# Optimization experiments

Hardware: AMD Instinct MI355X
Metric: run time of the kernel (lower is better)

The kernel has to match this reference:

```python
import jax, jax.numpy as jnp
import numpy as np

SR = 16000; NFFT = 1024; HOP = 256; NMELS = 80; GRUH = 256; ZDIM = 16
NBINS = 65; HID = 512; B = 8; TLEN = 160000; PAD = NFFT // 2; IRLEN = 8000

def _consts():
    freqs = np.linspace(0, SR / 2, NFFT // 2 + 1); fsq = freqs ** 2
    aw = (12194.217 ** 2 * fsq ** 2) / ((fsq + 20.6 ** 2) * (fsq + 107.7 ** 2) * (fsq + 737.9 ** 2) * (fsq + 12194.217 ** 2) ** 0.5 + 1e-8)
    h2m = lambda f: 2595.0 * np.log10(1.0 + f / 700.0)
    m2h = lambda m: 700.0 * (10.0 ** (m / 2595.0) - 1.0)
    f_pts = m2h(np.linspace(h2m(0.0), h2m(SR / 2.0), NMELS + 2))
    fd = f_pts[1:] - f_pts[:-1]
    sl = f_pts[None, :] - freqs[:, None]
    fb = np.maximum(0.0, np.minimum(-sl[:, :-2] / fd[:-1], sl[:, 2:] / fd[1:]))
    win = 0.5 - 0.5 * np.cos(2.0 * np.pi * np.arange(NFFT) / NFFT)  # periodic hann
    return jnp.asarray(aw, jnp.float32), jnp.asarray(fb, jnp.float32), jnp.asarray(win, jnp.float32)
AW, MELFB, WIN = _consts()

def _frame(x, size, hop):
    n = (x.shape[-1] - size) // hop + 1
    idx = jnp.arange(n)[:, None] * hop + jnp.arange(size)[None, :]
    return x[:, idx]

def _stft(x):  # [B,T] -> [B, n_frames, 513] complex
    xp = jnp.pad(x, ((0, 0), (PAD, PAD)), mode='reflect')
    return jnp.fft.rfft(_frame(xp, NFFT, HOP) * WIN, axis=-1)

def _istft(spec, length):  # [B, n_frames, 513] -> [B, length]
    fr = jnp.fft.irfft(spec, n=NFFT, axis=-1) * WIN
    n = fr.shape[1]; total = (n - 1) * HOP + NFFT
    idx = (jnp.arange(n)[:, None] * HOP + jnp.arange(NFFT)[None, :]).reshape(-1)
    out = jnp.zeros((fr.shape[0], total), fr.dtype).at[:, idx].add(fr.reshape(fr.shape[0], -1))
    wsq = jnp.zeros((total,), WIN.dtype).at[idx].add(jnp.tile(WIN ** 2, (n,)))
    out = out / jnp.where(wsq > 1e-11, wsq, 1.0)
    return out[:, PAD:PAD + length]

def _lin_interp(x, size):  # torch F.interpolate(mode='linear', align_corners=False) on last axis
    L = x.shape[-1]
    pos = jnp.clip((jnp.arange(size) + 0.5) * (L / size) - 0.5, 0.0, L - 1.0)
    lo = jnp.floor(pos).astype(jnp.int32); hi = jnp.minimum(lo + 1, L - 1); w = pos - lo
    return x[..., lo] * (1.0 - w) + x[..., hi] * w

def _gru(x, wih, whh, bih, bhh):  # torch nn.GRU, batch_first, h0=0
    xp = x @ wih.T + bih
    def step(h, xt):
        gh = h @ whh.T + bhh
        xr, xz, xn = jnp.split(xt, 3, -1); hr, hz, hn = jnp.split(gh, 3, -1)
        r = jax.nn.sigmoid(xr + hr); z = jax.nn.sigmoid(xz + hz)
        nn_ = jnp.tanh(xn + r * hn)
        h = (1.0 - z) * nn_ + z * h
        return h, h
    h0 = jnp.zeros((x.shape[0], whh.shape[1]), x.dtype)
    _, hs = jax.lax.scan(step, h0, jnp.swapaxes(xp, 0, 1))
    return jnp.swapaxes(hs, 0, 1)

def _forward(audio, gender, age, gru_wih, gru_whh, gru_bih, gru_bhh, proj_w, proj_b,
             w0, b0, g0, e0, w1, b1, g1, e1, w2, b2, g2, e2,
             oq_w, oq_b, vt_w, vt_b, nf_w, nf_b, ir):
    # --- pitch via autocorrelation ---
    xp = jnp.pad(audio, ((0, 0), (PAD, PAD)), mode='reflect')
    fr = _frame(xp, NFFT, HOP)
    ps = jnp.abs(jnp.fft.rfft(fr, n=2 * NFFT, axis=-1)) ** 2
    ac = jnp.fft.irfft(ps, n=2 * NFFT, axis=-1)[..., :NFFT]
    ac = ac / (ac[..., :1] + 1e-8)
    min_lag, max_lag = SR // 1000, SR // 50  # 16, 320
    reg = ac[..., min_lag:max_lag]
    mv = jnp.max(reg, -1); mi = jnp.argmax(reg, -1)
    f0 = SR / (mi.astype(jnp.float32) + min_lag + 1e-8)
    f0 = jnp.where(mv < 0.3, 0.0, f0)[..., None]  # [B,F,1]
    # --- loudness + mels ---
    spec = jnp.abs(_stft(audio)) ** 2  # [B,F,513]
    loud = 10.0 * jnp.log10(jnp.mean((spec + 1e-8) * AW, -1, keepdims=True))  # [B,F,1]
    mels = jnp.log(spec @ MELFB + 1e-5)  # [B,F,80]
    mels = (mels - mels.mean(1, keepdims=True)) / jnp.sqrt(mels.var(1, keepdims=True) + 1e-5)
    z = _gru(mels, gru_wih, gru_whh, gru_bih, gru_bhh) @ proj_w.T + proj_b  # [B,F,16]
    Fn = f0.shape[1]
    # --- controller ---
    gb = jnp.broadcast_to(gender[:, None, :], (gender.shape[0], Fn, 2))
    ab = jnp.broadcast_to(age[:, None, :], (age.shape[0], Fn, 1))
    h = jnp.concatenate([z, (jnp.log(f0 + 1e-5) - 4.0) / 4.0, loud / 100.0 + 1.0, gb, ab], -1)
    for W, bb, gm, bt in ((w0, b0, g0, e0), (w1, b1, g1, e1), (w2, b2, g2, e2)):
        h = h @ W.T + bb
        h = (h - h.mean(-1, keepdims=True)) / jnp.sqrt(h.var(-1, keepdims=True) + 1e-5) * gm + bt
        h = jnp.where(h >= 0, h, 0.1 * h)  # LeakyReLU(0.1)
    oq = jax.nn.sigmoid(h @ oq_w.T + oq_b)
    vt = jax.nn.sigmoid(h @ vt_w.T + vt_b)
    nf = jax.nn.sigmoid(h @ nf_w.T + nf_b)
    amp = 10.0 ** (loud / 20.0)
    # --- decoder ---
    L = audio.shape[-1]
    f0u = _lin_interp(f0[..., 0], L); ampu = _lin_interp(amp[..., 0], L); oqu = _lin_interp(oq[..., 0], L)
    phase = jnp.cumsum(f0u / SR, -1); p = phase - jnp.floor(phase)
    oqc = jnp.clip(oqu, 0.1, 0.9)
    pulse = 0.5 * (1.0 - jnp.cos(jnp.pi * p / (oqc + 1e-8)))
    g = pulse * jax.nn.sigmoid((oqc - p) * 100.0)
    glottal = jnp.pad(g[..., 1:] - g[..., :-1], ((0, 0), (1, 0)))
    noise = jax.random.normal(jax.random.key(42), glottal.shape, glottal.dtype)
    def apply_filter(ex, filt):
        es = _stft(ex)  # [B,nf,513]
        ft = _lin_interp(jnp.swapaxes(filt, 1, 2), es.shape[1])  # time interp
        ff = _lin_interp(jnp.swapaxes(ft, 1, 2), es.shape[2])    # bin interp 65->513
        return _istft(es * ff, L)
    dry = (apply_filter(glottal, vt) + apply_filter(noise, nf)) * ampu
    # --- FFT reverb ---
    nconv = int(2 ** int(np.ceil(np.log2(L + IRLEN - 1))))
    wet = jnp.fft.irfft(jnp.fft.rfft(dry, n=nconv) * jnp.fft.rfft(ir, n=nconv), n=nconv)[..., :L]
    return wet, dry

def setup_inputs() -> dict:
    ks = iter(jax.random.split(jax.random.key(0), 48))
    def nrm(shape, s=0.05):
        return jax.random.normal(next(ks), shape, jnp.float32) * s
    inp = {}
    inp['audio'] = jax.random.normal(next(ks), (B, TLEN), jnp.float32)
    inp['gender'] = jax.random.uniform(next(ks), (B, 2), jnp.float32)
    inp['age'] = jax.random.uniform(next(ks), (B, 1), jnp.float32)
    inp['gru_wih'] = nrm((3 * GRUH, NMELS)); inp['gru_whh'] = nrm((3 * GRUH, GRUH))
    inp['gru_bih'] = jnp.zeros((3 * GRUH,), jnp.float32); inp['gru_bhh'] = jnp.zeros((3 * GRUH,), jnp.float32)
    inp['proj_w'] = nrm((ZDIM, GRUH)); inp['proj_b'] = jnp.zeros((ZDIM,), jnp.float32)
    din = ZDIM + 5
    inp['w0'] = nrm((HID, din)); inp['b0'] = jnp.zeros((HID,), jnp.float32)
    inp['g0'] = jnp.ones((HID,), jnp.float32); inp['e0'] = jnp.zeros((HID,), jnp.float32)
    inp['w1'] = nrm((HID, HID)); inp['b1'] = jnp.zeros((HID,), jnp.float32)
    inp['g1'] = jnp.ones((HID,), jnp.float32); inp['e1'] = jnp.zeros((HID,), jnp.float32)
    inp['w2'] = nrm((HID, HID)); inp['b2'] = jnp.zeros((HID,), jnp.float32)
    inp['g2'] = jnp.ones((HID,), jnp.float32); inp['e2'] = jnp.zeros((HID,), jnp.float32)
    inp['oq_w'] = nrm((1, HID)); inp['oq_b'] = jnp.zeros((1,), jnp.float32)
    inp['vt_w'] = nrm((NBINS, HID)); inp['vt_b'] = jnp.zeros((NBINS,), jnp.float32)
    inp['nf_w'] = nrm((NBINS, HID)); inp['nf_b'] = jnp.zeros((NBINS,), jnp.float32)
    decay = jnp.exp(-jnp.linspace(0.0, 5.0, IRLEN))
    inp['ir'] = jax.random.normal(next(ks), (IRLEN,), jnp.float32) * 0.1 * decay
    return inp

def reference(audio, gender, age, gru_wih, gru_whh, gru_bih, gru_bhh, proj_w, proj_b,
              w0, b0, g0, e0, w1, b1, g1, e1, w2, b2, g2, e2,
              oq_w, oq_b, vt_w, vt_b, nf_w, nf_b, ir):
    return _forward(audio, gender, age, gru_wih, gru_whh, gru_bih, gru_bhh, proj_w, proj_b,
                    w0, b0, g0, e0, w1, b1, g1, e1, w2, b2, g2, e2,
                    oq_w, oq_b, vt_w, vt_b, nf_w, nf_b, ir)
```

## Files before the change

### kernel.cpp

```cpp
#include <hip/hip_runtime.h>
#include <math.h>

#define SRF 16000.0f
#define HOP 256
#define FRM 626
#define BB 8
#define TLEN 160000
#define NFRM (BB*FRM)
#define NCONV 262144
#define ACCLEN 161024
#define GCH 40

constexpr size_t oWIN   = 0;
constexpr size_t oTW    = oWIN + 1024;
constexpr size_t oDIAG  = oTW + 1024;
constexpr size_t oTWF   = oDIAG + 16;
constexpr size_t oTWC   = oTWF + 1024;
constexpr size_t oAW    = oTWC + 1024;
constexpr size_t oMELFB = oAW + 513;
constexpr size_t oWSQI  = oMELFB + 513*80;
constexpr size_t oWIHT  = oWSQI + ACCLEN;
constexpr size_t oW0T   = oWIHT + 80*768;
constexpr size_t oW1T   = oW0T + 21*512;
constexpr size_t oW2T   = oW1T + 512*512;
constexpr size_t oVTT   = oW2T + 512*512;
constexpr size_t oNFT   = oVTT + 512*65;
constexpr size_t oF0    = oNFT + 512*65;
constexpr size_t oLOUD  = oF0 + NFRM;
constexpr size_t oOQ    = oLOUD + NFRM;
constexpr size_t oVT    = oOQ + NFRM;
constexpr size_t oNF    = oVT + (size_t)NFRM*65;
constexpr size_t oGLOT  = oNF + (size_t)NFRM*65;
constexpr size_t oNOISE = oGLOT + (size_t)BB*TLEN;
constexpr size_t oACC   = oNOISE + (size_t)BB*TLEN;
constexpr size_t oCONVA = oACC + (size_t)BB*ACCLEN;
constexpr size_t oEND   = oCONVA + (size_t)9*NCONV*2;
constexpr size_t oXP    = oEND;
constexpr size_t oGSUM  = oXP + (size_t)NFRM*768;
constexpr size_t oGPRE  = oGSUM + 320;
constexpr size_t oEND2  = oGPRE + 640;
constexpr size_t oCONVB = oWSQI;
constexpr size_t oMEL = oCONVA;
constexpr size_t oHS  = oMEL + (size_t)NFRM*80;

constexpr long R_WIN=1024, R_TW=512, R_TWF=512, R_TWC=512, R_AW=513, R_MELFB=41040,
  R_WSQI=161024, R_WIHT=61440, R_W0T=10752, R_W1T=262144, R_W2T=262144,
  R_VTT=33280, R_NFT=33280, R_IR=NCONV;
constexpr long INIT_TOTAL = R_WIN+R_TW+R_TWF+R_TWC+R_AW+R_MELFB+R_WSQI+R_WIHT+R_W0T+
  R_W1T+R_W2T+R_VTT+R_NFT+R_IR;

constexpr int NOISEB = 313;
constexpr int ZACCB  = 315;
constexpr int MEGA_BLOCKS = 1 + NFRM + NOISEB + ZACCB;

typedef float f32x4 __attribute__((ext_vector_type(4)));
typedef __bf16 bf16x8 __attribute__((ext_vector_type(8)));
typedef short short8 __attribute__((ext_vector_type(8)));
#define MFMA_BF16 __builtin_amdgcn_mfma_f32_16x16x32_bf16

__device__ inline int mirror_idx(int j) {
  if (j < 0) j = -j;
  if (j >= TLEN) j = 2*TLEN - 2 - j;
  return j;
}
__device__ inline float sigm(float x) { return 1.0f/(1.0f + expf(-x)); }
__device__ inline unsigned short f2bf(float x) {
  unsigned u = __float_as_uint(x);
  return (unsigned short)((u + 0x7FFFu + ((u >> 16) & 1u)) >> 16);
}
__device__ inline float tanh_fast(float x) {
  return 1.0f - 2.0f/(__expf(2.0f*x) + 1.0f);
}

__device__ inline float interpF(const float* v, int i) {
  float pos = ((float)i + 0.5f) * (626.0f/160000.0f) - 0.5f;
  pos = fminf(fmaxf(pos, 0.0f), 625.0f);
  int lo = (int)floorf(pos);
  int hi = min(lo + 1, 625);
  float w = pos - (float)lo;
  return v[lo]*(1.0f - w) + v[hi]*w;
}
__device__ inline float interp65(const float* v, int k) {
  float pos = ((float)k + 0.5f) * (65.0f/513.0f) - 0.5f;
  pos = fminf(fmaxf(pos, 0.0f), 64.0f);
  int lo = (int)floorf(pos);
  int hi = min(lo + 1, 64);
  float w = pos - (float)lo;
  return v[lo]*(1.0f - w) + v[hi]*w;
}
__device__ inline float gwave(float ph, float oqu) {
  float p = ph - floorf(ph);
  float oqc = fminf(fmaxf(oqu, 0.1f), 0.9f);
  float pulse = 0.5f*(1.0f - cosf(3.14159265358979f * p / (oqc + 1e-8f)));
  float gs = 1.0f/(1.0f + __expf(-(oqc - p)*100.0f));
  return pulse*gs;
}

template<int LOGN, int TS>
__device__ inline void fft2(float2* c, const float2* tw, int tid, int nthr, bool inv) {
  constexpr int N = 1 << LOGN;
  for (int s = 1; s <= LOGN; ++s) {
    const int half = 1 << (s-1);
    const int tstep = (N >> s) * TS;
    for (int bf = tid; bf < (N>>1); bf += nthr) {
      int jj = bf & (half-1);
      int i0 = ((bf >> (s-1)) << s) + jj;
      int i1 = i0 + half;
      float2 wv = tw[jj*tstep];
      float wi = inv ? -wv.y : wv.y;
      float2 u = c[i0], v = c[i1];
      float tr  = v.x*wv.x - v.y*wi;
      float tci = v.x*wi  + v.y*wv.x;
      c[i0] = make_float2(u.x + tr, u.y + tci);
      c[i1] = make_float2(u.x - tr, u.y - tci);
    }
    __syncthreads();
  }
}

__device__ inline void threefry2x32(unsigned k0, unsigned k1, unsigned x0, unsigned x1,
                                    unsigned& o0, unsigned& o1) {
  unsigned ks2 = k0 ^ k1 ^ 0x1BD11BDAu;
  x0 += k0; x1 += k1;
#define TF_R(r) { x0 += x1; x1 = (x1<<(r)) | (x1>>(32-(r))); x1 ^= x0; }
  TF_R(13) TF_R(15) TF_R(26) TF_R(6)
  x0 += k1; x1 += ks2 + 1u;
  TF_R(17) TF_R(29) TF_R(16) TF_R(24)
  x0 += ks2; x1 += k0 + 2u;
  TF_R(13) TF_R(15) TF_R(26) TF_R(6)
  x0 += k0; x1 += k1 + 3u;
  TF_R(17) TF_R(29) TF_R(16) TF_R(24)
  x0 += k1; x1 += ks2 + 4u;
  TF_R(13) TF_R(15) TF_R(26) TF_R(6)
  x0 += ks2; x1 += k0 + 5u;
#undef TF_R
  o0 = x0; o1 = x1;
}

__device__ inline float erfinv_f(float x) {
  float w = -log1pf(-x*x);
  float p;
  if (w < 5.0f) {
    w = w - 2.5f;
    p = 2.81022636e-08f;
    p = fmaf(p, w, 3.43273939e-07f);
    p = fmaf(p, w, -3.5233877e-06f);
    p = fmaf(p, w, -4.39150654e-06f);
    p = fmaf(p, w, 0.00021858087f);
    p = fmaf(p, w, -0.00125372503f);
    p = fmaf(p, w, -0.00417768164f);
    p = fmaf(p, w, 0.246640727f);
    p = fmaf(p, w, 1.50140941f);
  } else {
    w = sqrtf(w) - 3.0f;
    p = -0.000200214257f;
    p = fmaf(p, w, 0.000100950558f);
    p = fmaf(p, w, 0.00134934322f);
    p = fmaf(p, w, -0.00367342844f);
    p = fmaf(p, w, 0.00573950773f);
    p = fmaf(p, w, -0.0076224613f);
    p = fmaf(p, w, 0.00943887047f);
    p = fmaf(p, w, 1.00167406f);
    p = fmaf(p, w, 2.83297682f);
  }
  return p*x;
}
__device__ inline float normal_from_bits(unsigned bits) {
  float f = __uint_as_float((bits >> 9) | 0x3F800000u) - 1.0f;
  float x = fmaxf(-0.99999994f, fmaf(f, 1.99999994f, -0.99999994f));
  return 1.41421356237f * erfinv_f(x);
}

__device__ inline double mel_fpt(int j) {
  double mmax = 2595.0 * log10(1.0 + 8000.0/700.0);
  return 700.0 * (pow(10.0, (mmax * (double)j / 81.0) / 2595.0) - 1.0);
}

__global__ void k_init(float* W, const float* wih, const float* w0,
                       const float* w1, const float* w2, const float* vtw, const float* nfw,
                       const float* ir) {
  long id = (long)blockIdx.x*256 + threadIdx.x;
  if (id < R_WIN) {
    double w = 0.5 - 0.5*cos(2.0*M_PI*(double)id/1024.0);
    W[oWIN+id] = (float)w; return;
  } id -= R_WIN;
  if (id < R_TW) {
    double a = -2.0*M_PI*(double)id/1024.0;
    W[oTW+2*id] = (float)cos(a); W[oTW+2*id+1] = (float)sin(a); return;
  } id -= R_TW;
  if (id < R_TWF) {
    double a = -2.0*M_PI*(double)id/262144.0;
    W[oTWF+2*id] = (float)cos(a); W[oTWF+2*id+1] = (float)sin(a); return;
  } id -= R_TWF;
  if (id < R_TWC) {
    double a = -2.0*M_PI*(double)id/512.0;
    W[oTWC+2*id] = (float)cos(a); W[oTWC+2*id+1] = (float)sin(a); return;
  } id -= R_TWC;
  if (id < R_AW) {
    double fr = (double)id*(8000.0/512.0); double fsq = fr*fr;
    double num = 12194.217*12194.217*fsq*fsq;
    double den = (fsq+20.6*20.6)*(fsq+107.7*107.7)*(fsq+737.9*737.9)*sqrt(fsq+12194.217*12194.217) + 1e-8;
    W[oAW+id] = (float)(num/den); return;
  } id -= R_AW;
  if (id < R_MELFB) {
    int k = (int)(id/80), m = (int)(id%80);
    double fk = (double)k*(8000.0/512.0);
    double f0p = mel_fpt(m), f1p = mel_fpt(m+1), f2p = mel_fpt(m+2);
    double lower = (fk - f0p)/(f1p - f0p);
    double upper = (f2p - fk)/(f2p - f1p);
    double v = fmax(0.0, fmin(lower, upper));
    W[oMELFB+id] = (float)v; return;
  } id -= R_MELFB;
  if (id < R_WSQI) {
    int t = (int)id;
    int n1 = t/256; if (n1 > 625) n1 = 625;
    int n0t = t - 1023 + 255; int n0 = (n0t > 0) ? n0t/256 : 0;
    double s = 0.0;
    for (int n = n0; n <= n1; ++n) {
      int o = t - n*256;
      double wv = 0.5 - 0.5*cos(2.0*M_PI*(double)o/1024.0);
      s += wv*wv;
    }
    float sf = (float)s;
    W[oWSQI+t] = (sf > 1e-11f) ? (1.0f/sf) : 1.0f; return;
  } id -= R_WSQI;
  if (id < R_WIHT) { long k = id/768, g = id%768; W[oWIHT+id] = wih[g*80+k];  return; } id -= R_WIHT;
  if (id < R_W0T)  { long d = id/512, j = id%512; W[oW0T+id] = w0[j*21+d];   return; } id -= R_W0T;
  if (id < R_W1T)  { long k = id/512, j = id%512; W[oW1T+id] = w1[j*512+k];  return; } id -= R_W1T;
  if (id < R_W2T)  { long k = id/512, j = id%512; W[oW2T+id] = w2[j*512+k];  return; } id -= R_W2T;
  if (id < R_VTT)  { long k = id/65,  m = id%65;  W[oVTT+id] = vtw[m*512+k]; return; } id -= R_VTT;
  if (id < R_NFT)  { long k = id/65,  m = id%65;  W[oNFT+id] = nfw[m*512+k]; return; } id -= R_NFT;
  if (id < R_IR) {
    size_t base = oCONVA + 2*((size_t)8*NCONV + id);
    W[base] = (id < 8000) ? ir[id] : 0.0f; W[base+1] = 0.0f; return;
  }
}

__global__ __launch_bounds__(256) void k_stft_mel(const float* audio, float* W) {
  int blk = blockIdx.x; int b = blk/FRM, f = blk%FRM; int tid = threadIdx.x;
  __shared__ float2 cb[1024];
  __shared__ float spec[513];
  __shared__ float redbuf[4];
  const float* arow = audio + (size_t)b*TLEN;
  const float2* tw = (const float2*)(W + oTW);
  for (int i = tid; i < 1024; i += 256) {
    float v = arow[mirror_idx(f*256 + i - 512)] * W[oWIN + i];
    int pos = __brev((unsigned)i) >> 22;
    cb[pos] = make_float2(v, 0.f);
  }
  __syncthreads();
  fft2<10,1>(cb, tw, tid, 256, false);
  for (int k = tid; k < 513; k += 256) { float2 z = cb[k]; spec[k] = z.x*z.x + z.y*z.y; }
  __syncthreads();
  float part = 0.f;
  for (int k = tid; k < 513; k += 256) part += (spec[k] + 1e-8f) * W[oAW + k];
  for (int off = 32; off; off >>= 1) part += __shfl_down(part, off, 64);
  if ((tid & 63) == 0) redbuf[tid >> 6] = part;
  __syncthreads();
  if (tid == 0) {
    float s = redbuf[0]+redbuf[1]+redbuf[2]+redbuf[3];
    W[oLOUD + blk] = 10.0f * log10f(s / 513.0f);
  }
  for (int m = tid; m < 80; m += 256) {
    float s = 0.f;
    for (int k = 0; k < 513; ++k) s += spec[k]*W[oMELFB + (size_t)k*80 + m];
    W[oMEL + (size_t)blk*80 + m] = logf(s + 1e-5f);
  }
}

__global__ void k_melnorm(float* W) {
  int id = blockIdx.x*256 + threadIdx.x;
  if (id >= BB*80) return;
  int b = id/80, m = id%80;
  double s = 0.0, ss = 0.0;
  for (int f = 0; f < FRM; ++f) {
    double v = W[oMEL + ((size_t)b*FRM + f)*80 + m];
    s += v; ss += v*v;
  }
  double mean = s/FRM;
  double var = ss/FRM - mean*mean;
  float mu = (float)mean;
  float rstd = (float)(1.0/sqrt(var + 1e-5));
  for (int f = 0; f < FRM; ++f) {
    size_t idx = oMEL + ((size_t)b*FRM + f)*80 + m;
    W[idx] = (W[idx] - mu)*rstd;
  }
}

__global__ void k_xp(float* W, const float* bih) {
  size_t id = (size_t)blockIdx.x*256 + threadIdx.x;
  if (id >= (size_t)NFRM*768) return;
  int g = (int)(id % 768);
  size_t q = id / 768;
  const float* mrow = W + oMEL + q*80;
  float acc = bih[g];
  for (int k = 0; k < 80; ++k) acc = fmaf(mrow[k], W[oWIHT + (size_t)k*768 + g], acc);
  W[oXP + q*768 + g] = acc;
}

__global__ __launch_bounds__(512, 2) void k_mega(float* W, const float* audio,
                                                 const float* whh, const float* bhh) {
  __shared__ unsigned short sB[32768];
  __shared__ unsigned short sA[4096];
  __shared__ float sGH[6144];
  __shared__ float fr4[4][1032];
  __shared__ float wpow[8];
  __shared__ float wmax[8];
  __shared__ int   wmaxi[8];
  int tid = threadIdx.x;
  int blk = blockIdx.x;

  if (blk == 0) {
    int w = tid >> 6, l = tid & 63;
    const float* XP = W + oXP;
    float* HS = W + oHS;

    for (int idx = tid; idx < 32768; idx += 512) {
      int lcol = idx >> 8, k = idx & 255;
      int gcol = 96*(lcol >> 4) + 80 + (lcol & 15);
      sB[lcol*256 + (k ^ ((lcol & 7) << 3))] = f2bf(whh[(size_t)gcol*256 + k]);
    }
    for (int idx = tid; idx < 4096; idx += 512) sA[idx] = 0;

    int cl = l & 15, khalf = (l >> 4) * 8;
    bf16x8 bw[40];
    #pragma unroll
    for (int t2 = 0; t2 < 5; ++t2) {
      int col = (6*w + t2)*16 + cl;
      #pragma unroll
      for (int kk = 0; kk < 8; ++kk) {
        const float* src = whh + (size_t)col*256 + kk*32 + khalf;
        short8 tmp;
        #pragma unroll
        for (int j = 0; j < 8; ++j) tmp[j] = (short)f2bf(src[j]);
        bw[t2*8 + kk] = __builtin_bit_cast(bf16x8, tmp);
      }
    }

    int g = tid & 255, bbase = tid >> 8;
    float bh_r = bhh[g], bh_z = bhh[256 + g], bh_n = bhh[512 + g];
    float hprev[4] = {0.f, 0.f, 0.f, 0.f};
    int aXor = (cl & 7) << 3;
    int lcol5 = w*16 + cl;

    float xrA[4], xzA[4], xnA[4];
    #pragma unroll
    for (int j = 0; j < 4; ++j) {
      const float* xpp = XP + ((size_t)(bbase + 2*j)*FRM + 0)*768 + g;
      xrA[j] = xpp[0]; xzA[j] = xpp[256]; xnA[j] = xpp[512];
    }

    __syncthreads();

#define LDA(kk) (*(const bf16x8*)&sA[(cl)*256 + (((kk)*32 + khalf) ^ aXor)])
#define LDB(kk) (*(const bf16x8*)&sB[(lcol5)*256 + (((kk)*32 + khalf) ^ aXor)])
#define STEPK(A_, kk) \
      c0 = MFMA_BF16(A_, bw[0*8+(kk)], c0, 0, 0, 0); \
      c1 = MFMA_BF16(A_, bw[1*8+(kk)], c1, 0, 0, 0); \
      c2 = MFMA_BF16(A_, bw[2*8+(kk)], c2, 0, 0, 0); \
      c3 = MFMA_BF16(A_, bw[3*8+(kk)], c3, 0, 0, 0); \
      c4 = MFMA_BF16(A_, bw[4*8+(kk)], c4, 0, 0, 0); \
      c5 = MFMA_BF16(A_, LDB(kk), c5, 0, 0, 0);

    for (int t = 0; t < FRM; ++t) {
      float xrB[4], xzB[4], xnB[4];
      int tn = (t + 1 < FRM) ? t + 1 : t;
      #pragma unroll
      for (int j = 0; j < 4; ++j) {
        const float* xpp = XP + ((size_t)(bbase + 2*j)*FRM + tn)*768 + g;
        xrB[j] = xpp[0]; xzB[j] = xpp[256]; xnB[j] = xpp[512];
      }
      f32x4 c0 = {0,0,0,0}, c1 = {0,0,0,0}, c2 = {0,0,0,0};
      f32x4 c3 = {0,0,0,0}, c4 = {0,0,0,0}, c5 = {0,0,0,0};
      bf16x8 a0 = LDA(0), a1 = LDA(1), a2 = LDA(2), a3 = LDA(3);
      STEPK(a0, 0) STEPK(a1, 1) STEPK(a2, 2) STEPK(a3, 3)
      a0 = LDA(4); a1 = LDA(5); a2 = LDA(6); a3 = LDA(7);
      STEPK(a0, 4) STEPK(a1, 5) STEPK(a2, 6) STEPK(a3, 7)
      int rowg = l >> 4;
      if (rowg < 2) {
        #pragma unroll
        for (int j = 0; j < 4; ++j) {
          int row = rowg*4 + j;
          sGH[row*768 + (6*w + 0)*16 + cl] = c0[j];
          sGH[row*768 + (6*w + 1)*16 + cl] = c1[j];
          sGH[row*768 + (6*w + 2)*16 + cl] = c2[j];
          sGH[row*768 + (6*w + 3)*16 + cl] = c3[j];
          sGH[row*768 + (6*w + 4)*16 + cl] = c4[j];
          sGH[row*768 + (6*w + 5)*16 + cl] = c5[j];
        }
      }
      __syncthreads();
      #pragma unroll
      for (int j = 0; j < 4; ++j) {
        int bb = bbase + 2*j;
        float ghr = sGH[bb*768 + g];
        float ghz = sGH[bb*768 + 256 + g];
        float ghn = sGH[bb*768 + 512 + g];
        float r = 1.0f/(1.0f + __expf(-(xrA[j] + ghr + bh_r)));
        float z = 1.0f/(1.0f + __expf(-(xzA[j] + ghz + bh_z)));
        float nn = tanh_fast(xnA[j] + r*(ghn + bh_n));
        float h = (1.0f - z)*nn + z*hprev[j];
        hprev[j] = h;
        HS[((size_t)bb*FRM + t)*256 + g] = h;
        sA[bb*256 + (g ^ ((bb & 7) << 3))] = f2bf(h);
      }
      __syncthreads();
      #pragma unroll
      for (int j = 0; j < 4; ++j) { xrA[j] = xrB[j]; xzA[j] = xzB[j]; xnA[j] = xnB[j]; }
    }
#undef LDA
#undef LDB
#undef STEPK
    return;
  }
  blk -= 1;

  if (blk < NFRM) {
    int b = blk/FRM, f = blk%FRM;
    const float* arow = audio + (size_t)b*TLEN;
    for (int idx = tid; idx < 4*1032; idx += 512) {
      int s = idx/1032, i = idx - s*1032;
      int j = i + s;
      fr4[s][i] = (j < 1024) ? arow[mirror_idx(f*256 + j - 512)] : 0.f;
    }
    __syncthreads();
    int lane = tid & 63, wv = tid >> 6;
    float p = 0.f;
    for (int i = tid; i < 1024; i += 512) { float x = fr4[0][i]; p += x*x; }
    for (int off = 32; off; off >>= 1) p += __shfl_down(p, off, 64);
    if (lane == 0) wpow[wv] = p;
    float vbest = -1e30f; int ibest = tid;
    if (tid < 304) {
      int lag = 16 + tid;
      int s = lag & 3, base = lag - s;
      int qmax = (1023 - lag) >> 2;
      float acc = 0.f;
      for (int q = 0; q <= qmax; ++q) {
        float4 u = *(const float4*)&fr4[0][4*q];
        float4 v = *(const float4*)&fr4[s][base + 4*q];
        acc += u.x*v.x + u.y*v.y + u.z*v.z + u.w*v.w;
      }
      vbest = acc;
    }
    for (int off = 32; off; off >>= 1) {
      float v2 = __shfl_down(vbest, off, 64);
      int i2 = __shfl_down(ibest, off, 64);
      if (v2 > vbest || (v2 == vbest && i2 < ibest)) { vbest = v2; ibest = i2; }
    }
    if (lane == 0) { wmax[wv] = vbest; wmaxi[wv] = ibest; }
    __syncthreads();
    if (tid == 0) {
      float ac0 = 0.f;
      #pragma unroll
      for (int q = 0; q < 8; ++q) ac0 += wpow[q];
      float bv = wmax[0]; int bi = wmaxi[0];
      #pragma unroll
      for (int q = 1; q < 8; ++q) {
        if (wmax[q] > bv || (wmax[q] == bv && wmaxi[q] < bi)) { bv = wmax[q]; bi = wmaxi[q]; }
      }
      float inv = 1.0f/(ac0 + 1e-8f);
      float best = bv*inv;
      W[oF0 + (size_t)blk] = (best < 0.3f) ? 0.0f : (SRF/(float)(bi + 16));
    }
    return;
  }
  blk -= NFRM;

  if (blk < NOISEB) {
    size_t base = (size_t)blk*4096;
    #pragma unroll
    for (int j = 0; j < 8; ++j) {
      size_t p = base + (size_t)j*512 + tid;
      if (p < (size_t)BB*TLEN) {
        unsigned o0, o1;
        threefry2x32(0u, 42u, 0u, (unsigned)p, o0, o1);
        W[oNOISE + p] = normal_from_bits(o0 ^ o1);
      }
    }
    return;
  }
  blk -= NOISEB;

  {
    size_t base = (size_t)blk*4096;
    #pragma unroll
    for (int j = 0; j < 8; ++j) {
      size_t p = base + (size_t)j*512 + tid;
      if (p < (size_t)BB*ACCLEN) W[oACC + p] = 0.0f;
    }
  }
}

__device__ inline void ln_lrelu(float acc[8], float gj, float ej, float out[8][512],
                                float wred[8][8][2], float stat[8][2],
                                int tid, int lane, int wv, int j) {
  #pragma unroll
  for (int i = 0; i < 8; ++i) {
    float s = acc[i], ss = acc[i]*acc[i];
    for (int off = 32; off; off >>= 1) { s += __shfl_down(s, off, 64); ss += __shfl_down(ss, off, 64); }
    if (lane == 0) { wred[i][wv][0] = s; wred[i][wv][1] = ss; }
  }
  __syncthreads();
  if (tid < 8) {
    float s = 0.f, ss = 0.f;
    #pragma unroll
    for (int w = 0; w < 8; ++w) { s += wred[tid][w][0]; ss += wred[tid][w][1]; }
    float mean = s/512.0f;
    float var = ss/512.0f - mean*mean;
    stat[tid][0] = mean;
    stat[tid][1] = 1.0f/sqrtf(var + 1e-5f);
  }
  __syncthreads();
  #pragma unroll
  for (int i = 0; i < 8; ++i) {
    float v = (acc[i] - stat[i][0])*stat[i][1]*gj + ej;
    out[i][j] = (v >= 0.f) ? v : 0.1f*v;
  }
}

__global__ __launch_bounds__(512) void k_mlp(float* W, const float* gender, const float* age,
    const float* projw, const float* projb,
    const float* b0, const float* g0, const float* e0,
    const float* b1, const float* g1, const float* e1,
    const float* b2, const float* g2, const float* e2,
    const float* oqw, const float* oqb, const float* vtb, const float* nfb) {
  __shared__ float hbuf[8][256];
  __shared__ float in0[8][21];
  __shared__ float actA[8][512];
  __shared__ float actB[8][512];
  __shared__ float wred[8][8][2];
  __shared__ float stat[8][2];
  int tid = threadIdx.x; int q0 = blockIdx.x*8;
  for (int x = tid; x < 2048; x += 512) {
    int i = x >> 8, k = x & 255;
    hbuf[i][k] = W[oHS + ((size_t)(q0 + i))*256 + k];
  }
  __syncthreads();
  if (tid < 128) {
    int i = tid >> 4, zi = tid & 15;
    float a = projb[zi];
    for (int k = 0; k < 256; ++k) a = fmaf(hbuf[i][k], projw[zi*256 + k], a);
    in0[i][zi] = a;
  } else if (tid < 168) {
    int x = tid - 128; int i = x/5, d = 16 + x%5;
    int q = q0 + i; int b = q/FRM;
    float v;
    if (d == 16) v = (logf(W[oF0 + q] + 1e-5f) - 4.0f)*0.25f;
    else if (d == 17) v = W[oLOUD + q]/100.0f + 1.0f;
    else if (d == 18) v = gender[b*2];
    else if (d == 19) v = gender[b*2 + 1];
    else v = age[b];
    in0[i][d] = v;
  }
  __syncthreads();
  int j = tid, lane = tid & 63, wv = tid >> 6;
  float acc[8];
  #pragma unroll
  for (int i = 0; i < 8; ++i) acc[i] = b0[j];
  for (int d = 0; d < 21; ++d) {
    float w = W[oW0T + (size_t)d*512 + j];
    #pragma unroll
    for (int i = 0; i < 8; ++i) acc[i] = fmaf(in0[i][d], w, acc[i]);
  }
  ln_lrelu(acc, g0[j], e0[j], actA, wred, stat, tid, lane, wv, j);
  __syncthreads();
  #pragma unroll
  for (int i = 0; i < 8; ++i) acc[i] = b1[j];
  for (int k = 0; k < 512; ++k) {
    float w = W[oW1T + (size_t)k*512 + j];
    #pragma unroll
    for (int i = 0; i < 8; ++i) acc[i] = fmaf(actA[i][k], w, acc[i]);
  }
  ln_lrelu(acc, g1[j], e1[j], actB, wred, stat, tid, lane, wv, j);
  __syncthreads();
  #pragma unroll
  for (int i = 0; i < 8; ++i) acc[i] = b2[j];
  for (int k = 0; k < 512; ++k) {
    float w = W[oW2T + (size_t)k*512 + j];
    #pragma unroll
    for (int i = 0; i < 8; ++i) acc[i] = fmaf(actB[i][k], w, acc[i]);
  }
  ln_lrelu(acc, g2[j], e2[j], actA, wred, stat, tid, lane, wv, j);
  __syncthreads();
  for (int x = tid; x < 520; x += 512) {
    int i = x/65, m = x%65;
    float a = vtb[m], a2 = nfb[m];
    for (int k = 0; k < 512; ++k) {
      float h = actA[i][k];
      a  = fmaf(h, W[oVTT + (size_t)k*65 + m], a);
      a2 = fmaf(h, W[oNFT + (size_t)k*65 + m], a2);
    }
    W[oVT + (size_t)(q0+i)*65 + m] = sigm(a);
    W[oNF + (size_t)(q0+i)*65 + m] = sigm(a2);
  }
  if (tid < 8) {
    float a = oqb[0];
    for (int k = 0; k < 512; ++k) a = fmaf(actA[tid][k], oqw[k], a);
    W[oOQ + q0 + tid] = sigm(a);
  }
}

__global__ __launch_bounds__(256) void k_gsum(float* W) {
  int blk = blockIdx.x; int b = blk/GCH, c = blk%GCH; int tid = threadIdx.x;
  __shared__ float ws[4];
  const float* f0r = W + oF0 + (size_t)b*FRM;
  int i0 = c*4096 + tid*16;
  float s = 0.f;
  #pragma unroll
  for (int j = 0; j < 16; ++j) {
    int i = i0 + j;
    if (i < TLEN) s += interpF(f0r, i)*(1.0f/SRF);
  }
  for (int off = 32; off; off >>= 1) s += __shfl_down(s, off, 64);
  if ((tid & 63) == 0) ws[tid >> 6] = s;
  __syncthreads();
  if (tid == 0) W[oGSUM + (size_t)b*GCH + c] = ws[0]+ws[1]+ws[2]+ws[3];
}

__global__ void k_gscan(float* W) {
  if (blockIdx.x == 0 && threadIdx.x == 0) {
    double* P = (double*)(W + oGPRE);
    for (int b = 0; b < BB; ++b) {
      double a = 0.0;
      for (int c = 0; c < GCH; ++c) {
        P[b*GCH + c] = a;
        a += (double)W[oGSUM + (size_t)b*GCH + c];
      }
    }
  }
}

__global__ __launch_bounds__(256) void k_gapply(float* W) {
  int blk = blockIdx.x; int b = blk/GCH, c = blk%GCH; int tid = threadIdx.x;
  __shared__ float wss[4];
  __shared__ float lastw[4];
  const float* f0r = W + oF0 + (size_t)b*FRM;
  const float* oqr = W + oOQ + (size_t)b*FRM;
  float* grow = W + oGLOT + (size_t)b*TLEN;
  double P = ((const double*)(W + oGPRE))[b*GCH + c];
  int i0 = c*4096 + tid*16;
  int lane = tid & 63, wv = tid >> 6;
  float v[16]; float ts = 0.f;
  #pragma unroll
  for (int j = 0; j < 16; ++j) {
    int i = i0 + j;
    float x = (i < TLEN) ? interpF(f0r, i)*(1.0f/SRF) : 0.f;
    v[j] = x; ts += x;
  }
  float sc = ts;
  #pragma unroll
  for (int off = 1; off < 64; off <<= 1) {
    float o = __shfl_up(sc, off, 64);
    if (lane >= off) sc += o;
  }
  if (lane == 63) wss[wv] = sc;
  __syncthreads();
  float wpre = 0.f;
  for (int q = 0; q < wv; ++q) wpre += wss[q];
  double ph0 = P + (double)(wpre + sc - ts);
  float run = 0.f; float gq[16];
  #pragma unroll
  for (int j = 0; j < 16; ++j) {
    int i = i0 + j;
    run += v[j];
    float ph = (float)(ph0 + (double)run);
    gq[j] = gwave(ph, interpF(oqr, min(i, TLEN-1)));
  }
  float prev = __shfl_up(gq[15], 1, 64);
  if (lane == 63) lastw[wv] = gq[15];
  __syncthreads();
  if (lane == 0) {
    if (wv > 0) prev = lastw[wv - 1];
    else if (i0 > 0) prev = gwave((float)P, interpF(oqr, i0 - 1));
    else prev = 0.f;
  }
  #pragma unroll
  for (int j = 0; j < 16; ++j) {
    int i = i0 + j;
    if (i < TLEN) {
      float gl = (j == 0) ? prev : gq[j-1];
      grow[i] = (i == 0) ? 0.f : (gq[j] - gl);
    }
  }
}

__global__ __launch_bounds__(256) void k_filtsynth(float* W) {
  int blk = blockIdx.x; int b = blk/FRM, f = blk%FRM; int tid = threadIdx.x;
  __shared__ float2 cG[1024], cN[1024];
  __shared__ float fvt[65], fnf[65];
  const float* grow = W + oGLOT + (size_t)b*TLEN;
  const float* nrow = W + oNOISE + (size_t)b*TLEN;
  const float2* tw = (const float2*)(W + oTW);
  for (int i = tid; i < 1024; i += 256) {
    int si = mirror_idx(f*256 + i - 512);
    float wv = W[oWIN + i];
    int pos = __brev((unsigned)i) >> 22;
    cG[pos] = make_float2(grow[si]*wv, 0.f);
    cN[pos] = make_float2(nrow[si]*wv, 0.f);
  }
  if (tid < 65) {
    fvt[tid] = W[oVT + ((size_t)b*FRM + f)*65 + tid];
    fnf[tid] = W[oNF + ((size_t)b*FRM + f)*65 + tid];
  }
  __syncthreads();
  fft2<10,1>(cG, tw, tid, 256, false);
  fft2<10,1>(cN, tw, tid, 256, false);
  for (int k = tid; k < 1024; k += 256) {
    int kp = min(k, 1024 - k);
    float fv = interp65(fvt, kp);
    float fn = interp65(fnf, kp);
    float2 zg = cG[k], zn = cN[k];
    cG[k] = make_float2(zg.x*fv + zn.x*fn, zg.y*fv + zn.y*fn);
  }
  __syncthreads();
  for (int i = tid; i < 1024; i += 256) {
    int jj = __brev((unsigned)i) >> 22;
    if (jj > i) { float2 t2 = cG[i]; cG[i] = cG[jj]; cG[jj] = t2; }
  }
  __syncthreads();
  fft2<10,1>(cG, tw, tid, 256, true);
  float* arow = W + oACC + (size_t)b*ACCLEN + (size_t)f*256;
  for (int i = tid; i < 1024; i += 256) {
    float xv = cG[i].x*(1.0f/1024.0f)*W[oWIN + i];
    atomicAdd(arow + i, xv);
  }
}

__global__ void k_dry(float* W, float* dout) {
  size_t id = (size_t)blockIdx.x*256 + threadIdx.x;
  if (id >= (size_t)BB*NCONV) return;
  int b = (int)(id / NCONV);
  int n = (int)(id % NCONV);
  float dv = 0.f;
  if (n < TLEN) {
    float val = W[oACC + (size_t)b*ACCLEN + 512 + n] * W[oWSQI + 512 + n];
    const float* lrow = W + oLOUD + (size_t)b*FRM;
    float pos = ((float)n + 0.5f) * (626.0f/160000.0f) - 0.5f;
    pos = fminf(fmaxf(pos, 0.0f), 625.0f);
    int lo = (int)floorf(pos);
    int hi = min(lo + 1, 625);
    float w = pos - (float)lo;
    float a0 = exp10f(lrow[lo]*0.05f);
    float a1 = exp10f(lrow[hi]*0.05f);
    float ampu = a0*(1.0f - w) + a1*w;
    dv = val*ampu;
    dout[(size_t)BB*TLEN + (size_t)b*TLEN + n] = dv;
  }
  ((float2*)(W + oCONVA))[id] = make_float2(dv, 0.f);
}

__global__ __launch_bounds__(256) void k_conv_f1(const float* in, float* out,
                                                 const float* tw, const float* twf,
                                                 const float* twc) {
  int blk = blockIdx.x; int t = blk >> 9; int bcol = blk & 511; int tid = threadIdx.x;
  __shared__ float2 cb[512];
  const float2* src = (const float2*)in + (size_t)t*NCONV;
  for (int a = tid; a < 512; a += 256) {
    int pos = __brev((unsigned)a) >> 23;
    cb[pos] = src[(size_t)a*512 + bcol];
  }
  __syncthreads();
  fft2<9,2>(cb, (const float2*)tw, tid, 256, false);
  float2* dst = (float2*)out + (size_t)t*NCONV + (size_t)bcol*512;
  for (int k1 = tid; k1 < 512; k1 += 256) {
    unsigned m = (unsigned)bcol * (unsigned)k1;
    float2 tc = ((const float2*)twc)[m >> 9];
    float2 tf = ((const float2*)twf)[m & 511];
    float wr = tc.x*tf.x - tc.y*tf.y;
    float wi = tc.x*tf.y + tc.y*tf.x;
    float2 v = cb[k1];
    dst[k1] = make_float2(v.x*wr - v.y*wi, v.x*wi + v.y*wr);
  }
}

__global__ __launch_bounds__(256) void k_conv_f2(const float* in, float* out, const float* tw) {
  int blk = blockIdx.x; int t = blk >> 9; int k1 = blk & 511; int tid = threadIdx.x;
  __shared__ float2 cb[512];
  const float2* src = (const float2*)in + (size_t)t*NCONV;
  for (int bb2 = tid; bb2 < 512; bb2 += 256) {
    int pos = __brev((unsigned)bb2) >> 23;
    cb[pos] = src[(size_t)bb2*512 + k1];
  }
  __syncthreads();
  fft2<9,2>(cb, (const float2*)tw, tid, 256, false);
  float2* dst = (float2*)out + (size_t)t*NCONV;
  for (int k2 = tid; k2 < 512; k2 += 256) {
    dst[(size_t)k1 + 512*(size_t)k2] = cb[k2];
  }
}

__global__ void k_mul(float* W) {
  size_t id = (size_t)blockIdx.x*256 + threadIdx.x;
  if (id >= (size_t)BB*NCONV) return;
  size_t k = id % NCONV;
  float2* A = (float2*)(W + oCONVA);
  float2 a = A[id];
  float2 c = A[(size_t)8*NCONV + k];
  float pr = a.x*c.x - a.y*c.y;
  float pi = a.x*c.y + a.y*c.x;
  A[id] = make_float2(pr, -pi);
}

__global__ void k_wet(const float* W, float* dout) {
  size_t id = (size_t)blockIdx.x*256 + threadIdx.x;
  if (id >= (size_t)BB*TLEN) return;
  size_t b = id / TLEN, n = id % TLEN;
  dout[id] = ((const float2*)(W + oCONVA))[b*NCONV + n].x * (1.0f/262144.0f);
}

extern "C" void kernel_launch(void* const* d_in, const int* in_sizes, int n_in,
                              void* d_out, int out_size, void* d_ws, size_t ws_size,
                              hipStream_t stream) {
  (void)in_sizes; (void)n_in; (void)out_size; (void)ws_size;
  const float* audio  = (const float*)d_in[0];
  const float* gender = (const float*)d_in[1];
  const float* age    = (const float*)d_in[2];
  const float* wih    = (const float*)d_in[3];
  const float* whh    = (const float*)d_in[4];
  const float* bih    = (const float*)d_in[5];
  const float* bhh    = (const float*)d_in[6];
  const float* projw  = (const float*)d_in[7];
  const float* projb  = (const float*)d_in[8];
  const float* w0     = (const float*)d_in[9];
  const float* b0     = (const float*)d_in[10];
  const float* g0     = (const float*)d_in[11];
  const float* e0     = (const float*)d_in[12];
  const float* w1     = (const float*)d_in[13];
  const float* b1     = (const float*)d_in[14];
  const float* g1     = (const float*)d_in[15];
  const float* e1     = (const float*)d_in[16];
  const float* w2     = (const float*)d_in[17];
  const float* b2     = (const float*)d_in[18];
  const float* g2     = (const float*)d_in[19];
  const float* e2     = (const float*)d_in[20];
  const float* oqw    = (const float*)d_in[21];
  const float* oqb    = (const float*)d_in[22];
  const float* vtw    = (const float*)d_in[23];
  const float* vtb    = (const float*)d_in[24];
  const float* nfw    = (const float*)d_in[25];
  const float* nfb    = (const float*)d_in[26];
  const float* ir     = (const float*)d_in[27];
  float* W = (float*)d_ws;
  float* dout = (float*)d_out;

  k_init<<<(int)((INIT_TOTAL + 255)/256), 256, 0, stream>>>(W, wih, w0, w1, w2, vtw, nfw, ir);
  k_stft_mel<<<NFRM, 256, 0, stream>>>(audio, W);
  k_melnorm<<<3, 256, 0, stream>>>(W);
  k_xp<<<(int)(((size_t)NFRM*768 + 255)/256), 256, 0, stream>>>(W, bih);
  k_mega<<<MEGA_BLOCKS, 512, 0, stream>>>(W, audio, whh, bhh);
  k_mlp<<<NFRM/8, 512, 0, stream>>>(W, gender, age, projw, projb,
                                    b0, g0, e0, b1, g1, e1, b2, g2, e2, oqw, oqb, vtb, nfb);
  k_gsum<<<BB*GCH, 256, 0, stream>>>(W);
  k_gscan<<<1, 64, 0, stream>>>(W);
  k_gapply<<<BB*GCH, 256, 0, stream>>>(W);
  k_filtsynth<<<NFRM, 256, 0, stream>>>(W);
  k_dry<<<(int)(((size_t)BB*NCONV + 255)/256), 256, 0, stream>>>(W, dout);
  k_conv_f1<<<9*512, 256, 0, stream>>>(W + oCONVA, W + oCONVB, W + oTW, W + oTWF, W + oTWC);
  k_conv_f2<<<9*512, 256, 0, stream>>>(W + oCONVB, W + oCONVA, W + oTW);
  k_mul<<<(int)(((size_t)BB*NCONV + 255)/256), 256, 0, stream>>>(W);
  k_conv_f1<<<8*512, 256, 0, stream>>>(W + oCONVA, W + oCONVB, W + oTW, W + oTWF, W + oTWC);
  k_conv_f2<<<8*512, 256, 0, stream>>>(W + oCONVB, W + oCONVA, W + oTW);
  k_wet<<<(int)(((size_t)BB*TLEN + 255)/256), 256, 0, stream>>>(W, dout);
}
```

Measured before the change: 2.462 ms.

## Transpose GRU gate scratch for vector LDS access and sparsify mel filterbank loop

The recurrent GRU block now writes MFMA accumulators as whole f32x4 vectors into a transposed gate buffer and reads each thread's four batch rows with single vector loads. Batch rows are regrouped so each thread owns four consecutive batches, and the weight column mapping changes to match. The input-projection prefetch for the next timestep is removed, so those loads are now issued within the same step. Separately, the mel projection loops only over each filter's nonzero frequency range instead of all 513 bins, relying on a mel_fpt helper whose bounds must exactly cover the filter support.

```diff
diff --git a/kernel.cpp b/kernel.cpp
--- a/kernel.cpp
+++ b/kernel.cpp
@@ -262,8 +262,11 @@
     W[oLOUD + blk] = 10.0f * log10f(s / 513.0f);
   }
   for (int m = tid; m < 80; m += 256) {
+    double f0p = mel_fpt(m), f2p = mel_fpt(m + 2);
+    int klo = (int)(f0p * (512.0/8000.0)); if (klo < 0) klo = 0;
+    int khi = (int)(f2p * (512.0/8000.0)) + 1; if (khi > 512) khi = 512;
     float s = 0.f;
-    for (int k = 0; k < 513; ++k) s += spec[k]*W[oMELFB + (size_t)k*80 + m];
+    for (int k = klo; k <= khi; ++k) s += spec[k]*W[oMELFB + (size_t)k*80 + m];
     W[oMEL + (size_t)blk*80 + m] = logf(s + 1e-5f);
   }
 }
@@ -302,7 +305,7 @@
                                                  const float* whh, const float* bhh) {
   __shared__ unsigned short sB[32768];
   __shared__ unsigned short sA[4096];
-  __shared__ float sGH[6144];
+  __shared__ float sGT[9216];
   __shared__ float fr4[4][1032];
   __shared__ float wpow[8];
   __shared__ float wmax[8];
@@ -326,7 +329,7 @@
     bf16x8 bw[40];
     #pragma unroll
     for (int t2 = 0; t2 < 5; ++t2) {
-      int col = (6*w + t2)*16 + cl;
+      int col = 96*w + 16*t2 + cl;
       #pragma unroll
       for (int kk = 0; kk < 8; ++kk) {
         const float* src = whh + (size_t)col*256 + kk*32 + khalf;
@@ -342,13 +345,12 @@
     float hprev[4] = {0.f, 0.f, 0.f, 0.f};
     int aXor = (cl & 7) << 3;
     int lcol5 = w*16 + cl;
-
-    float xrA[4], xzA[4], xnA[4];
-    #pragma unroll
-    for (int j = 0; j < 4; ++j) {
-      const float* xpp = XP + ((size_t)(bbase + 2*j)*FRM + 0)*768 + g;
-      xrA[j] = xpp[0]; xzA[j] = xpp[256]; xnA[j] = xpp[512];
-    }
+    int rowg = l >> 4;
+    int colb = 96*w + cl;
+    int gtw = colb*12 + rowg*4;
+    int gtr0 = g*12 + 4*bbase;
+    int gtr1 = (256 + g)*12 + 4*bbase;
+    int gtr2 = (512 + g)*12 + 4*bbase;
 
     __syncthreads();
 
@@ -363,12 +365,11 @@
       c5 = MFMA_BF16(A_, LDB(kk), c5, 0, 0, 0);
 
     for (int t = 0; t < FRM; ++t) {
-      float xrB[4], xzB[4], xnB[4];
-      int tn = (t + 1 < FRM) ? t + 1 : t;
+      float xr[4], xz[4], xn[4];
       #pragma unroll
       for (int j = 0; j < 4; ++j) {
-        const float* xpp = XP + ((size_t)(bbase + 2*j)*FRM + tn)*768 + g;
-        xrB[j] = xpp[0]; xzB[j] = xpp[256]; xnB[j] = xpp[512];
+        const float* xpp = XP + ((size_t)(4*bbase + j)*FRM + t)*768 + g;
+        xr[j] = xpp[0]; xz[j] = xpp[256]; xn[j] = xpp[512];
       }
       f32x4 c0 = {0,0,0,0}, c1 = {0,0,0,0}, c2 = {0,0,0,0};
       f32x4 c3 = {0,0,0,0}, c4 = {0,0,0,0}, c5 = {0,0,0,0};
@@ -376,37 +377,30 @@
       STEPK(a0, 0) STEPK(a1, 1) STEPK(a2, 2) STEPK(a3, 3)
       a0 = LDA(4); a1 = LDA(5); a2 = LDA(6); a3 = LDA(7);
       STEPK(a0, 4) STEPK(a1, 5) STEPK(a2, 6) STEPK(a3, 7)
-      int rowg = l >> 4;
-      if (rowg < 2) {
-        #pragma unroll
-        for (int j = 0; j < 4; ++j) {
-          int row = rowg*4 + j;
-          sGH[row*768 + (6*w + 0)*16 + cl] = c0[j];
-          sGH[row*768 + (6*w + 1)*16 + cl] = c1[j];
-          sGH[row*768 + (6*w + 2)*16 + cl] = c2[j];
-          sGH[row*768 + (6*w + 3)*16 + cl] = c3[j];
-          sGH[row*768 + (6*w + 4)*16 + cl] = c4[j];
-          sGH[row*768 + (6*w + 5)*16 + cl] = c5[j];
-        }
+      if (rowg < 3) {
+        *(f32x4*)&sGT[gtw + 0*192]  = c0;
+        *(f32x4*)&sGT[gtw + 1*192]  = c1;
+        *(f32x4*)&sGT[gtw + 2*192]  = c2;
+        *(f32x4*)&sGT[gtw + 3*192]  = c3;
+        *(f32x4*)&sGT[gtw + 4*192]  = c4;
+        *(f32x4*)&sGT[gtw + 5*192]  = c5;
       }
       __syncthreads();
+      f32x4 rv = *(const f32x4*)&sGT[gtr0];
+      f32x4 zv = *(const f32x4*)&sGT[gtr1];
+      f32x4 nv = *(const f32x4*)&sGT[gtr2];
       #pragma unroll
       for (int j = 0; j < 4; ++j) {
-        int bb = bbase + 2*j;
-        float ghr = sGH[bb*768 + g];
-        float ghz = sGH[bb*768 + 256 + g];
-        float ghn = sGH[bb*768 + 512 + g];
-        float r = 1.0f/(1.0f + __expf(-(xrA[j] + ghr + bh_r)));
-        float z = 1.0f/(1.0f + __expf(-(xzA[j] + ghz + bh_z)));
-        float nn = tanh_fast(xnA[j] + r*(ghn + bh_n));
+        int bb = 4*bbase + j;
+        float r = 1.0f/(1.0f + __expf(-(xr[j] + rv[j] + bh_r)));
+        float z = 1.0f/(1.0f + __expf(-(xz[j] + zv[j] + bh_z)));
+        float nn = tanh_fast(xn[j] + r*(nv[j] + bh_n));
         float h = (1.0f - z)*nn + z*hprev[j];
         hprev[j] = h;
         HS[((size_t)bb*FRM + t)*256 + g] = h;
         sA[bb*256 + (g ^ ((bb & 7) << 3))] = f2bf(h);
       }
       __syncthreads();
-      #pragma unroll
-      for (int j = 0; j < 4; ++j) { xrA[j] = xrB[j]; xzA[j] = xzB[j]; xnA[j] = xnB[j]; }
     }
 #undef LDA
 #undef LDB
```

Result: faster. 2.229 ms (-9.4%).
